# Kernel tuning notes

Measured on AMD Instinct MI355X. Metric: run time of the kernel, lower is better.

Reference implementation:

```python
import jax, jax.numpy as jnp
import numpy as np

BN_EPS = 1e-5

def setup_inputs() -> dict:
    key = jax.random.key(0)
    k1, k2, k3 = jax.random.split(key, 3)
    N, F, H, E = 50000, 256, 256, 1600000
    x = jax.random.normal(k1, (N, F), dtype=jnp.float32)
    edge_index = jax.random.randint(k2, (2, E), 0, N, dtype=jnp.int64)
    # Linear(F, H) params, PyTorch default init scale
    lim = 1.0 / np.sqrt(F)
    W = jax.random.uniform(k3, (H, F), dtype=jnp.float32, minval=-lim, maxval=lim)
    b = jnp.zeros((H,), dtype=jnp.float32)
    bn_w = jnp.ones((H,), dtype=jnp.float32)
    bn_b = jnp.zeros((H,), dtype=jnp.float32)
    return {"x": x, "edge_index": edge_index, "W": W, "b": b, "bn_w": bn_w, "bn_b": bn_b}

def reference(x, edge_index, W, b, bn_w, bn_b):
    N = x.shape[0]
    src, dst = edge_index[0], edge_index[1]
    # GIN aggregation: sum of neighbor features (messages flow src -> dst)
    agg = jax.ops.segment_sum(x[src], dst, num_segments=N)
    h = x + agg  # (1 + eps) * x + agg, eps = 0
    # MLP: Linear then BatchNorm1d (training mode: batch stats, biased var)
    h = jnp.einsum('nf,hf->nh', h, W) + b
    mean = jnp.mean(h, axis=0)
    var = jnp.mean(jnp.square(h - mean), axis=0)
    out = (h - mean) * jax.lax.rsqrt(var + BN_EPS) * bn_w + bn_b
    return out
```

## Files before the change

### kernel.cpp

```cpp
#include <hip/hip_runtime.h>

#define NN 50000
#define FDIM 256
#define HDIM 256
#define BN_EPS 1e-5f
#define RB 32
#define KC 16
#define NP 264
#define SCAN_CHUNK 1024
#define NBLK_SCAN ((NN + SCAN_CHUNK - 1) / SCAN_CHUNK)

#define BKT 32
#define NBKT 1563
#define ECAP 1280
#define CAP 1280
#define SBUF3 13000
#define NFB_MIN 128
#define PSC_NPT 7
#define PAIR_SRC(p) (((p) >> 5) & 0xFFFFu)
#define PAIR_LDST(p) ((p) & 31u)

typedef __attribute__((ext_vector_type(8))) short short8v;
typedef __attribute__((ext_vector_type(8))) unsigned short ushort8v;
typedef __attribute__((ext_vector_type(4))) float f32x4;

__device__ __forceinline__ float b2f(unsigned short u) {
    return __uint_as_float(((unsigned)u) << 16);
}
__device__ __forceinline__ unsigned short f2b(float f) {
    unsigned u = __float_as_uint(f);
    return (unsigned short)((u + 0x7FFFu + ((u >> 16) & 1u)) >> 16);
}

__launch_bounds__(256)
__global__ void k_cvtfill3(const float4* __restrict__ x, const float4* __restrict__ W,
                           ushort4* __restrict__ xb, ushort4* __restrict__ Wb,
                           int nx4, int nw4,
                           const int* __restrict__ src, const int* __restrict__ dst,
                           int* __restrict__ bcnt, unsigned int* __restrict__ pairs,
                           int E, int nfb) {
    const int bid = blockIdx.x;
    const int t = threadIdx.x;
    if (bid >= nfb) {
        int i = (bid - nfb) * 256 + t;
        if (i < nx4) {
            float4 v = x[i];
            xb[i] = make_ushort4(f2b(v.x), f2b(v.y), f2b(v.z), f2b(v.w));
        } else {
            int j = i - nx4;
            if (j < nw4) {
                float4 v = W[j];
                Wb[j] = make_ushort4(f2b(v.x), f2b(v.y), f2b(v.z), f2b(v.w));
            }
        }
        return;
    }
    __shared__ int lhist[NBKT];
    __shared__ int lofs[NBKT];
    __shared__ int ts[256];
    __shared__ unsigned int sbuf[SBUF3];
    const int chunk = (E + nfb - 1) / nfb;
    const int c0 = bid * chunk;
    const int c1 = min(E, c0 + chunk);
    const int n = c1 - c0;

    for (int i = t; i < NBKT; i += 256) lhist[i] = 0;
    __syncthreads();
    for (int e = c0 + t; e < c1; e += 256) atomicAdd(&lhist[dst[e] >> 5], 1);
    __syncthreads();
    {
        int i0 = t * PSC_NPT;
        int s = 0;
        int loc[PSC_NPT];
        for (int i = 0; i < PSC_NPT; i++) {
            int idx = i0 + i;
            loc[i] = (idx < NBKT) ? lhist[idx] : 0;
            s += loc[i];
        }
        ts[t] = s;
        __syncthreads();
        for (int off = 1; off < 256; off <<= 1) {
            int val = (t >= off) ? ts[t - off] : 0;
            __syncthreads();
            ts[t] += val;
            __syncthreads();
        }
        int run = ts[t] - s;
        for (int i = 0; i < PSC_NPT; i++) {
            int idx = i0 + i;
            if (idx < NBKT) {
                lofs[idx] = run;
                run += loc[i];
            }
        }
    }
    __syncthreads();
    for (int i = t; i < NBKT; i += 256) lhist[i] = lofs[i];
    __syncthreads();
    for (int e = c0 + t; e < c1; e += 256) {
        int d = dst[e];
        unsigned bkt = (unsigned)d >> 5;
        int rank = atomicAdd(&lhist[bkt], 1);
        sbuf[rank] = (bkt << 21) | ((unsigned)src[e] << 5) | ((unsigned)d & 31u);
    }
    __syncthreads();
    for (int i = t; i < NBKT; i += 256) {
        int cnt = lhist[i] - lofs[i];
        int gb = cnt ? (i * CAP + atomicAdd(&bcnt[i], cnt)) : 0;
        lhist[i] = gb - lofs[i];
    }
    __syncthreads();
    for (int j = t; j < n; j += 256) {
        unsigned int p = sbuf[j];
        unsigned bkt = p >> 21;
        int pos = j + lhist[bkt];
        if (pos < (int)((bkt + 1) * CAP)) pairs[pos] = p;
    }
}

__launch_bounds__(256, 6)
__global__ void k_agg_gemm(const ushort4* __restrict__ xb4, const unsigned int* __restrict__ pairs,
                           const int* __restrict__ bcnt,
                           const int* __restrict__ srcv, const int* __restrict__ dstv, int E,
                           const unsigned short* __restrict__ Wb, const float* __restrict__ bias,
                           unsigned short* __restrict__ hb, float* __restrict__ stat) {
    __shared__ unsigned int lp[ECAP];
    __shared__ int lhist[BKT];
    __shared__ int lofs[BKT + 1];
    __shared__ unsigned short As[BKT * NP];
    __shared__ float ssum[HDIM];
    __shared__ float ssq[HDIM];
    const int t = threadIdx.x;
    const int lane = t & 63;
    const int wid = t >> 6;
    const int q = lane >> 4;
    const int l16 = lane & 15;
    const int v0 = blockIdx.x * BKT;
    const int ebeg = blockIdx.x * CAP;
    const int ecnt = bcnt[blockIdx.x];
    const int vrows = min(BKT, NN - v0);

    ssum[t] = 0.f;
    ssq[t] = 0.f;

    if (ecnt <= ECAP) {
        if (t < BKT) lhist[t] = 0;
        __syncthreads();
        for (int e = t; e < ecnt; e += 256)
            atomicAdd(&lhist[PAIR_LDST(pairs[ebeg + e])], 1);
        __syncthreads();
        if (t == 0) {
            int run = 0;
            for (int r = 0; r < BKT; r++) { lofs[r] = run; run += lhist[r]; }
            lofs[BKT] = run;
        }
        __syncthreads();
        if (t < BKT) lhist[t] = lofs[t];
        __syncthreads();
        for (int e = t; e < ecnt; e += 256) {
            unsigned int p = pairs[ebeg + e];
            int pos = atomicAdd(&lhist[PAIR_LDST(p)], 1);
            lp[pos] = p;
        }
        __syncthreads();
#pragma unroll
        for (int i = 0; i < 8; i++) {
            int r = wid * 8 + i;
            int v = v0 + r;
            if (v < NN) {
                ushort4 u0 = xb4[(size_t)v * 64 + lane];
                float a0 = b2f(u0.x), a1 = b2f(u0.y), a2 = b2f(u0.z), a3 = b2f(u0.w);
                int e0 = __builtin_amdgcn_readfirstlane(lofs[r]);
                int e1 = __builtin_amdgcn_readfirstlane(lofs[r + 1]);
                int e = e0;
                for (; e + 16 <= e1; e += 16) {
                    ushort4 u[16];
#pragma unroll
                    for (int j = 0; j < 16; j++)
                        u[j] = xb4[(size_t)PAIR_SRC(lp[e + j]) * 64 + lane];
#pragma unroll
                    for (int j = 0; j < 16; j++) {
                        a0 += b2f(u[j].x); a1 += b2f(u[j].y);
                        a2 += b2f(u[j].z); a3 += b2f(u[j].w);
                    }
                }
                for (; e + 4 <= e1; e += 4) {
                    ushort4 ua = xb4[(size_t)PAIR_SRC(lp[e]) * 64 + lane];
                    ushort4 ub = xb4[(size_t)PAIR_SRC(lp[e + 1]) * 64 + lane];
                    ushort4 uc = xb4[(size_t)PAIR_SRC(lp[e + 2]) * 64 + lane];
                    ushort4 ud = xb4[(size_t)PAIR_SRC(lp[e + 3]) * 64 + lane];
                    a0 += (b2f(ua.x) + b2f(ub.x)) + (b2f(uc.x) + b2f(ud.x));
                    a1 += (b2f(ua.y) + b2f(ub.y)) + (b2f(uc.y) + b2f(ud.y));
                    a2 += (b2f(ua.z) + b2f(ub.z)) + (b2f(uc.z) + b2f(ud.z));
                    a3 += (b2f(ua.w) + b2f(ub.w)) + (b2f(uc.w) + b2f(ud.w));
                }
                for (; e < e1; e++) {
                    ushort4 ua = xb4[(size_t)PAIR_SRC(lp[e]) * 64 + lane];
                    a0 += b2f(ua.x); a1 += b2f(ua.y); a2 += b2f(ua.z); a3 += b2f(ua.w);
                }
                *(ushort4*)(As + r * NP + lane * 4) =
                    make_ushort4(f2b(a0), f2b(a1), f2b(a2), f2b(a3));
            } else {
                *(ushort4*)(As + r * NP + lane * 4) = make_ushort4(0, 0, 0, 0);
            }
        }
    } else {
#pragma unroll
        for (int i = 0; i < 8; i++) {
            int r = wid * 8 + i;
            int v = v0 + r;
            float a0 = 0.f, a1 = 0.f, a2 = 0.f, a3 = 0.f;
            if (v < NN) {
                ushort4 u0 = xb4[(size_t)v * 64 + lane];
                a0 = b2f(u0.x); a1 = b2f(u0.y); a2 = b2f(u0.z); a3 = b2f(u0.w);
                for (int e = 0; e < E; e++) {
                    if (dstv[e] == v) {
                        ushort4 cu = xb4[(size_t)srcv[e] * 64 + lane];
                        a0 += b2f(cu.x); a1 += b2f(cu.y); a2 += b2f(cu.z); a3 += b2f(cu.w);
                    }
                }
            }
            *(ushort4*)(As + r * NP + lane * 4) =
                make_ushort4(f2b(a0), f2b(a1), f2b(a2), f2b(a3));
        }
    }
    __syncthreads();

    f32x4 acc[2][4];
#pragma unroll
    for (int mt = 0; mt < 2; mt++)
#pragma unroll
        for (int nt = 0; nt < 4; nt++) acc[mt][nt] = (f32x4)0.f;

    const int w = wid;
#pragma unroll
    for (int ks = 0; ks < 8; ks++) {
        const int kk = ks * 32;
        short8v af[2], bf_[4];
#pragma unroll
        for (int mt = 0; mt < 2; mt++)
            af[mt] = *(const short8v*)(As + (mt * 16 + l16) * NP + kk + q * 8);
#pragma unroll
        for (int nt = 0; nt < 4; nt++)
            bf_[nt] = *(const short8v*)(Wb + (size_t)(w * 64 + nt * 16 + l16) * FDIM + kk + q * 8);
#pragma unroll
        for (int mt = 0; mt < 2; mt++)
#pragma unroll
            for (int nt = 0; nt < 4; nt++)
                acc[mt][nt] = __builtin_amdgcn_mfma_f32_16x16x32_bf16(af[mt], bf_[nt], acc[mt][nt], 0, 0, 0);
    }

#pragma unroll
    for (int nt = 0; nt < 4; nt++) {
        const int col = w * 64 + nt * 16 + l16;
        const float bcol = bias[col];
        float s = 0.f, qq = 0.f;
#pragma unroll
        for (int mt = 0; mt < 2; mt++) {
            const int rbase = mt * 16 + q * 4;
#pragma unroll
            for (int r = 0; r < 4; r++) {
                int row = rbase + r;
                if (row < vrows) {
                    float v = acc[mt][nt][r] + bcol;
                    hb[(size_t)(v0 + row) * FDIM + col] = f2b(v);
                    s += v;
                    qq += v * v;
                }
            }
        }
        atomicAdd(&ssum[col], s);
        atomicAdd(&ssq[col], qq);
    }
    __syncthreads();
    atomicAdd(&stat[t], ssum[t]);
    atomicAdd(&stat[256 + t], ssq[t]);
}

__global__ void k_norm8f(const ushort8v* __restrict__ hb8, const float* __restrict__ stat,
                         const float* __restrict__ bn_w, const float* __restrict__ bn_b,
                         float4* __restrict__ out, int n8) {
    __shared__ float ss[512];
    const int t = threadIdx.x;
    {
        const float inv_n = 1.0f / (float)NN;
        float mean = stat[t] * inv_n;
        float var = stat[256 + t] * inv_n - mean * mean;
        float sc = bn_w[t] * rsqrtf(var + BN_EPS);
        ss[t] = sc;
        ss[256 + t] = bn_b[t] - mean * sc;
    }
    __syncthreads();
    int i = blockIdx.x * 256 + t;
    if (i >= n8) return;
    ushort8v u = hb8[i];
    int c8 = (i & 31) << 3;
    float4 sc0 = *(const float4*)(ss + c8);
    float4 sc1 = *(const float4*)(ss + c8 + 4);
    float4 sh0 = *(const float4*)(ss + 256 + c8);
    float4 sh1 = *(const float4*)(ss + 256 + c8 + 4);
    float4 v0, v1;
    v0.x = fmaf(b2f(u[0]), sc0.x, sh0.x);
    v0.y = fmaf(b2f(u[1]), sc0.y, sh0.y);
    v0.z = fmaf(b2f(u[2]), sc0.z, sh0.z);
    v0.w = fmaf(b2f(u[3]), sc0.w, sh0.w);
    v1.x = fmaf(b2f(u[4]), sc1.x, sh1.x);
    v1.y = fmaf(b2f(u[5]), sc1.y, sh1.y);
    v1.z = fmaf(b2f(u[6]), sc1.z, sh1.z);
    v1.w = fmaf(b2f(u[7]), sc1.w, sh1.w);
    out[i * 2 + 0] = v0;
    out[i * 2 + 1] = v1;
}

__global__ void k_final(const float* __restrict__ stat, const float* __restrict__ bn_w,
                        const float* __restrict__ bn_b, float* __restrict__ ss) {
    int j = threadIdx.x;
    const float inv_n = 1.0f / (float)NN;
    float mean = stat[j] * inv_n;
    float var = stat[256 + j] * inv_n - mean * mean;
    float sc = bn_w[j] * rsqrtf(var + BN_EPS);
    ss[j] = sc;
    ss[256 + j] = bn_b[j] - mean * sc;
}
__global__ void k_hist(const int* __restrict__ dst, int* __restrict__ cnt, int E) {
    int e = blockIdx.x * blockDim.x + threadIdx.x;
    if (e < E) atomicAdd(&cnt[dst[e]], 1);
}
__global__ void k_scan1(const int* __restrict__ cnt, int* __restrict__ offs,
                        int* __restrict__ bsum) {
    __shared__ int ts[256];
    int t = threadIdx.x;
    int base = blockIdx.x * SCAN_CHUNK + t * 4;
    int v0 = (base + 0 < NN) ? cnt[base + 0] : 0;
    int v1 = (base + 1 < NN) ? cnt[base + 1] : 0;
    int v2 = (base + 2 < NN) ? cnt[base + 2] : 0;
    int v3 = (base + 3 < NN) ? cnt[base + 3] : 0;
    int tsum = v0 + v1 + v2 + v3;
    ts[t] = tsum;
    __syncthreads();
    for (int off = 1; off < 256; off <<= 1) {
        int val = (t >= off) ? ts[t - off] : 0;
        __syncthreads();
        ts[t] += val;
        __syncthreads();
    }
    int excl = ts[t] - tsum;
    if (t == 255) bsum[blockIdx.x] = ts[255];
    if (base + 0 < NN) offs[base + 0] = excl;
    if (base + 1 < NN) offs[base + 1] = excl + v0;
    if (base + 2 < NN) offs[base + 2] = excl + v0 + v1;
    if (base + 3 < NN) offs[base + 3] = excl + v0 + v1 + v2;
}
__global__ void k_scan2(int* __restrict__ bsum, int nb) {
    __shared__ int s[64];
    int t = threadIdx.x;
    s[t] = (t < nb) ? bsum[t] : 0;
    __syncthreads();
    if (t == 0) {
        int run = 0;
        for (int i = 0; i < nb; i++) { int v = s[i]; s[i] = run; run += v; }
    }
    __syncthreads();
    if (t < nb) bsum[t] = s[t];
}
__global__ void k_scan3(int* __restrict__ offs, const int* __restrict__ bsum,
                        int* __restrict__ cursor) {
    int i = blockIdx.x * blockDim.x + threadIdx.x;
    if (i >= NN) return;
    int o = offs[i] + bsum[i >> 10];
    offs[i] = o;
    cursor[i] = o;
}
__global__ void k_bucket(const int* __restrict__ src, const int* __restrict__ dst,
                         int* __restrict__ cursor, int* __restrict__ csr, int E) {
    int e = blockIdx.x * blockDim.x + threadIdx.x;
    if (e >= E) return;
    int pos = atomicAdd(&cursor[dst[e]], 1);
    csr[pos] = src[e];
}
__global__ void k_copy(const float4* __restrict__ x, float4* __restrict__ out, int n4) {
    int i = blockIdx.x * blockDim.x + threadIdx.x;
    if (i < n4) out[i] = x[i];
}
__global__ void k_scatter(const float* __restrict__ x, const int* __restrict__ src,
                          const int* __restrict__ dst, float* __restrict__ out, int E) {
    int t = blockIdx.x * blockDim.x + threadIdx.x;
    int e = t >> 6;
    if (e >= E) return;
    int c = (t & 63) << 2;
    long s = src[e], d = dst[e];
    const float4 v = *(const float4*)(x + s * FDIM + c);
    float* o = out + d * FDIM + c;
    atomicAdd(o + 0, v.x);
    atomicAdd(o + 1, v.y);
    atomicAdd(o + 2, v.z);
    atomicAdd(o + 3, v.w);
}
__launch_bounds__(256)
__global__ void k_gather(const float4* __restrict__ x, const int* __restrict__ offs,
                         const int* __restrict__ cnt, const int* __restrict__ csr,
                         float4* __restrict__ out) {
    int v = blockIdx.x * 4 + (threadIdx.x >> 6);
    if (v >= NN) return;
    int lane = threadIdx.x & 63;
    int beg = __builtin_amdgcn_readfirstlane(offs[v]);
    int d   = __builtin_amdgcn_readfirstlane(cnt[v]);
    float4 acc = x[(size_t)v * 64 + lane];
    int i = 0;
    for (; i + 4 <= d; i += 4) {
        int s0 = csr[beg + i], s1 = csr[beg + i + 1];
        int s2 = csr[beg + i + 2], s3 = csr[beg + i + 3];
        float4 a = x[(size_t)s0 * 64 + lane];
        float4 b = x[(size_t)s1 * 64 + lane];
        float4 c = x[(size_t)s2 * 64 + lane];
        float4 e = x[(size_t)s3 * 64 + lane];
        acc.x += (a.x + b.x) + (c.x + e.x);
        acc.y += (a.y + b.y) + (c.y + e.y);
        acc.z += (a.z + b.z) + (c.z + e.z);
        acc.w += (a.w + b.w) + (c.w + e.w);
    }
    for (; i < d; i++) {
        int s = csr[beg + i];
        float4 a = x[(size_t)s * 64 + lane];
        acc.x += a.x; acc.y += a.y; acc.z += a.z; acc.w += a.w;
    }
    out[(size_t)v * 64 + lane] = acc;
}
__launch_bounds__(256)
__global__ void k_gemm_stats(float* __restrict__ h,
                             const float* __restrict__ W,
                             const float* __restrict__ bias,
                             float* __restrict__ stat) {
    __shared__ float hs[RB * FDIM];
    __shared__ float wt[KC * HDIM];
    const int j = threadIdx.x;
    const int c = j & 63;
    const int g = j >> 6;
    const long row0 = (long)blockIdx.x * RB;
    const int vrows = min(RB, NN - (int)row0);
    const int vf4 = vrows * (FDIM / 4);

    float4* hsv = (float4*)hs;
    const float4* hv = (const float4*)(h + row0 * FDIM);
#pragma unroll
    for (int i = 0; i < (RB * FDIM / 4) / 256; i++) {
        int f4 = j + i * 256;
        hsv[f4] = (f4 < vf4) ? hv[f4] : make_float4(0.f, 0.f, 0.f, 0.f);
    }
    __syncthreads();

    float acc[8][4];
#pragma unroll
    for (int r = 0; r < 8; r++)
#pragma unroll
        for (int qi = 0; qi < 4; qi++) acc[r][qi] = 0.f;

    for (int kb = 0; kb < FDIM; kb += KC) {
        __syncthreads();
#pragma unroll
        for (int i = 0; i < KC / 4; i++) {
            float4 w4 = *(const float4*)(W + (size_t)j * FDIM + kb + i * 4);
            wt[(i * 4 + 0) * HDIM + j] = w4.x;
            wt[(i * 4 + 1) * HDIM + j] = w4.y;
            wt[(i * 4 + 2) * HDIM + j] = w4.z;
            wt[(i * 4 + 3) * HDIM + j] = w4.w;
        }
        __syncthreads();
#pragma unroll
        for (int k = 0; k < KC; k++) {
            float4 wv = *(const float4*)(wt + k * HDIM + c * 4);
#pragma unroll
            for (int r = 0; r < 8; r++) {
                float hval = hs[(g * 8 + r) * FDIM + kb + k];
                acc[r][0] = fmaf(hval, wv.x, acc[r][0]);
                acc[r][1] = fmaf(hval, wv.y, acc[r][1]);
                acc[r][2] = fmaf(hval, wv.z, acc[r][2]);
                acc[r][3] = fmaf(hval, wv.w, acc[r][3]);
            }
        }
    }
    __syncthreads();
    wt[j] = 0.f;
    wt[256 + j] = 0.f;
    __syncthreads();

    float4 bv = *(const float4*)(bias + c * 4);
    float s0 = 0, s1 = 0, s2 = 0, s3 = 0, q0 = 0, q1 = 0, q2 = 0, q3 = 0;
#pragma unroll
    for (int r = 0; r < 8; r++) {
        int row = g * 8 + r;
        if (row < vrows) {
            float4 v;
            v.x = acc[r][0] + bv.x;
            v.y = acc[r][1] + bv.y;
            v.z = acc[r][2] + bv.z;
            v.w = acc[r][3] + bv.w;
            *(float4*)(h + (row0 + row) * FDIM + c * 4) = v;
            s0 += v.x; s1 += v.y; s2 += v.z; s3 += v.w;
            q0 += v.x * v.x; q1 += v.y * v.y; q2 += v.z * v.z; q3 += v.w * v.w;
        }
    }
    atomicAdd(&wt[c * 4 + 0], s0);
    atomicAdd(&wt[c * 4 + 1], s1);
    atomicAdd(&wt[c * 4 + 2], s2);
    atomicAdd(&wt[c * 4 + 3], s3);
    atomicAdd(&wt[256 + c * 4 + 0], q0);
    atomicAdd(&wt[256 + c * 4 + 1], q1);
    atomicAdd(&wt[256 + c * 4 + 2], q2);
    atomicAdd(&wt[256 + c * 4 + 3], q3);
    __syncthreads();
    atomicAdd(&stat[j], wt[j]);
    atomicAdd(&stat[256 + j], wt[256 + j]);
}
__global__ void k_norm(float* __restrict__ out, const float* __restrict__ ss, int n4) {
    int i = blockIdx.x * blockDim.x + threadIdx.x;
    if (i >= n4) return;
    float4 v = ((float4*)out)[i];
    int c4 = (i & 63) << 2;
    float4 sc = *(const float4*)(ss + c4);
    float4 sh = *(const float4*)(ss + 256 + c4);
    v.x = fmaf(v.x, sc.x, sh.x);
    v.y = fmaf(v.y, sc.y, sh.y);
    v.z = fmaf(v.z, sc.z, sh.z);
    v.w = fmaf(v.w, sc.w, sh.w);
    ((float4*)out)[i] = v;
}

extern "C" void kernel_launch(void* const* d_in, const int* in_sizes, int n_in,
                              void* d_out, int out_size, void* d_ws, size_t ws_size,
                              hipStream_t stream) {
    const float* x   = (const float*)d_in[0];
    const int*   ei  = (const int*)d_in[1];
    const float* W   = (const float*)d_in[2];
    const float* b   = (const float*)d_in[3];
    const float* bnw = (const float*)d_in[4];
    const float* bnb = (const float*)d_in[5];
    float* out = (float*)d_out;
    char* ws = (char*)d_ws;
    const int E = in_sizes[1] / 2;
    const int n4 = NN * FDIM / 4;
    const int n8 = NN * FDIM / 8;
    const int* src = ei;
    const int* dst = ei + E;

    size_t off = 0;
    float* stat = (float*)(ws + off);          off += 4096;
    int* bcnt   = (int*)(ws + off);            off += 8192;
    unsigned int* pairs = (unsigned int*)(ws + off); off += (size_t)NBKT * CAP * 4;
    off = (off + 255) & ~(size_t)255;
    unsigned short* Wb = (unsigned short*)(ws + off); off += 131072;
    unsigned short* xb = (unsigned short*)(ws + off); off += (size_t)NN * FDIM * 2;
    unsigned short* hb = (unsigned short*)(ws + off); off += (size_t)NN * FDIM * 2;
    const size_t need_fast = off;

    size_t foff = 0;
    float* fstat  = (float*)(ws + foff); foff += 4096;
    int*   cnt    = (int*)(ws + foff);   foff += 204800;
    int*   offs   = (int*)(ws + foff);   foff += 204800;
    int*   cursor = (int*)(ws + foff);   foff += 204800;
    int*   bsum   = (int*)(ws + foff);   foff += 4096;
    int*   csr    = (int*)(ws + foff);   foff += (size_t)E * 4;
    const size_t need_mid = foff;

    const bool src_fits = (NN <= 65536);
    const int nw4 = HDIM * FDIM / 4;

    if (ws_size >= need_fast && src_fits) {
        hipMemsetAsync(ws, 0, 12288, stream);
        int nfb = (E + SBUF3 - 1) / SBUF3;
        if (nfb < NFB_MIN) nfb = NFB_MIN;
        const int ncvt = (n4 + nw4 + 255) / 256;
        k_cvtfill3<<<nfb + ncvt, 256, 0, stream>>>((const float4*)x, (const float4*)W,
                                                   (ushort4*)xb, (ushort4*)Wb, n4, nw4,
                                                   src, dst, bcnt, pairs, E, nfb);
        k_agg_gemm<<<NBKT, 256, 0, stream>>>((const ushort4*)xb, pairs, bcnt,
                                             src, dst, E, Wb, b, hb, stat);
        k_norm8f<<<(n8 + 255) / 256, 256, 0, stream>>>((const ushort8v*)hb, stat,
                                                       bnw, bnb, (float4*)out, n8);
    } else if (ws_size >= need_mid) {
        hipMemsetAsync(fstat, 0, 2 * 256 * sizeof(float), stream);
        hipMemsetAsync(cnt, 0, NN * sizeof(int), stream);
        k_hist<<<(E + 255) / 256, 256, 0, stream>>>(dst, cnt, E);
        k_scan1<<<NBLK_SCAN, 256, 0, stream>>>(cnt, offs, bsum);
        k_scan2<<<1, 64, 0, stream>>>(bsum, NBLK_SCAN);
        k_scan3<<<(NN + 255) / 256, 256, 0, stream>>>(offs, bsum, cursor);
        k_bucket<<<(E + 255) / 256, 256, 0, stream>>>(src, dst, cursor, csr, E);
        k_gather<<<(NN + 3) / 4, 256, 0, stream>>>((const float4*)x, offs, cnt, csr,
                                                   (float4*)out);
        k_gemm_stats<<<(NN + RB - 1) / RB, 256, 0, stream>>>(out, W, b, fstat);
        k_final<<<1, 256, 0, stream>>>(fstat, bnw, bnb, fstat + 512);
        k_norm<<<(n4 + 255) / 256, 256, 0, stream>>>(out, fstat + 512, n4);
    } else {
        hipMemsetAsync(fstat, 0, 2 * 256 * sizeof(float), stream);
        k_copy<<<(n4 + 255) / 256, 256, 0, stream>>>((const float4*)x, (float4*)out, n4);
        long threads = (long)E * 64;
        k_scatter<<<(int)((threads + 255) / 256), 256, 0, stream>>>(x, src, dst, out, E);
        k_gemm_stats<<<(NN + RB - 1) / RB, 256, 0, stream>>>(out, W, b, fstat);
        k_final<<<1, 256, 0, stream>>>(fstat, bnw, bnb, fstat + 512);
        k_norm<<<(n4 + 255) / 256, 256, 0, stream>>>(out, fstat + 512, n4);
    }
}
```

Measured before the change: 320.4 us.

## Split edge bucketing into two halves and overlap second half with aggregation

```diff
diff --git a/kernel.cpp b/kernel.cpp
--- a/kernel.cpp
+++ b/kernel.cpp
@@ -12,11 +12,12 @@
 
 #define BKT 32
 #define NBKT 1563
+#define NBH 782
 #define ECAP 1280
 #define CAP 1280
-#define SBUF3 13000
-#define NFB_MIN 128
-#define PSC_NPT 7
+#define SBUF2 3200
+#define NFB_MIN 512
+#define SMEM_INTS 6144
 #define PAIR_SRC(p) (((p) >> 5) & 0xFFFFu)
 #define PAIR_LDST(p) ((p) & 31u)
 
@@ -32,49 +33,37 @@
     return (unsigned short)((u + 0x7FFFu + ((u >> 16) & 1u)) >> 16);
 }
 
-__launch_bounds__(256)
-__global__ void k_cvtfill3(const float4* __restrict__ x, const float4* __restrict__ W,
-                           ushort4* __restrict__ xb, ushort4* __restrict__ Wb,
-                           int nx4, int nw4,
-                           const int* __restrict__ src, const int* __restrict__ dst,
-                           int* __restrict__ bcnt, unsigned int* __restrict__ pairs,
-                           int E, int nfb) {
-    const int bid = blockIdx.x;
+__device__ __forceinline__ void fill_range(int cid, int nfb, int* smem,
+                                           const int* __restrict__ src,
+                                           const int* __restrict__ dst,
+                                           int* __restrict__ bcnt,
+                                           unsigned int* __restrict__ pairs,
+                                           int E, int bkt_lo, int bkt_hi) {
+    int* lhist = smem;
+    int* lofs  = smem + 800;
+    int* ts    = smem + 1600;
+    unsigned int* sbuf = (unsigned int*)(smem + 1856);
     const int t = threadIdx.x;
-    if (bid >= nfb) {
-        int i = (bid - nfb) * 256 + t;
-        if (i < nx4) {
-            float4 v = x[i];
-            xb[i] = make_ushort4(f2b(v.x), f2b(v.y), f2b(v.z), f2b(v.w));
-        } else {
-            int j = i - nx4;
-            if (j < nw4) {
-                float4 v = W[j];
-                Wb[j] = make_ushort4(f2b(v.x), f2b(v.y), f2b(v.z), f2b(v.w));
-            }
-        }
-        return;
-    }
-    __shared__ int lhist[NBKT];
-    __shared__ int lofs[NBKT];
-    __shared__ int ts[256];
-    __shared__ unsigned int sbuf[SBUF3];
+    const int nbh = bkt_hi - bkt_lo;
     const int chunk = (E + nfb - 1) / nfb;
-    const int c0 = bid * chunk;
+    const int c0 = cid * chunk;
     const int c1 = min(E, c0 + chunk);
-    const int n = c1 - c0;
-
-    for (int i = t; i < NBKT; i += 256) lhist[i] = 0;
-    __syncthreads();
-    for (int e = c0 + t; e < c1; e += 256) atomicAdd(&lhist[dst[e] >> 5], 1);
-    __syncthreads();
+
+    for (int i = t; i < nbh; i += 256) lhist[i] = 0;
+    __syncthreads();
+    for (int e = c0 + t; e < c1; e += 256) {
+        int b = dst[e] >> 5;
+        if (b >= bkt_lo && b < bkt_hi) atomicAdd(&lhist[b - bkt_lo], 1);
+    }
+    __syncthreads();
+    int ntot;
     {
-        int i0 = t * PSC_NPT;
+        int i0 = t * 4;
         int s = 0;
-        int loc[PSC_NPT];
-        for (int i = 0; i < PSC_NPT; i++) {
+        int loc[4];
+        for (int i = 0; i < 4; i++) {
             int idx = i0 + i;
-            loc[i] = (idx < NBKT) ? lhist[idx] : 0;
+            loc[i] = (idx < nbh) ? lhist[idx] : 0;
             s += loc[i];
         }
         ts[t] = s;
@@ -86,58 +75,66 @@
             __syncthreads();
         }
         int run = ts[t] - s;
-        for (int i = 0; i < PSC_NPT; i++) {
+        for (int i = 0; i < 4; i++) {
             int idx = i0 + i;
-            if (idx < NBKT) {
+            if (idx < nbh) {
                 lofs[idx] = run;
                 run += loc[i];
             }
         }
-    }
-    __syncthreads();
-    for (int i = t; i < NBKT; i += 256) lhist[i] = lofs[i];
+        ntot = ts[255];
+    }
+    __syncthreads();
+    for (int i = t; i < nbh; i += 256) lhist[i] = lofs[i];
     __syncthreads();
     for (int e = c0 + t; e < c1; e += 256) {
         int d = dst[e];
-        unsigned bkt = (unsigned)d >> 5;
-        int rank = atomicAdd(&lhist[bkt], 1);
-        sbuf[rank] = (bkt << 21) | ((unsigned)src[e] << 5) | ((unsigned)d & 31u);
-    }
-    __syncthreads();
-    for (int i = t; i < NBKT; i += 256) {
+        int b = d >> 5;
+        if (b >= bkt_lo && b < bkt_hi) {
+            unsigned bl = (unsigned)(b - bkt_lo);
+            int rank = atomicAdd(&lhist[bl], 1);
+            sbuf[rank] = (bl << 21) | ((unsigned)src[e] << 5) | ((unsigned)d & 31u);
+        }
+    }
+    __syncthreads();
+    for (int i = t; i < nbh; i += 256) {
         int cnt = lhist[i] - lofs[i];
-        int gb = cnt ? (i * CAP + atomicAdd(&bcnt[i], cnt)) : 0;
+        int gb = cnt ? ((bkt_lo + i) * CAP + atomicAdd(&bcnt[bkt_lo + i], cnt)) : 0;
         lhist[i] = gb - lofs[i];
     }
     __syncthreads();
-    for (int j = t; j < n; j += 256) {
+    for (int j = t; j < ntot; j += 256) {
         unsigned int p = sbuf[j];
-        unsigned bkt = p >> 21;
-        int pos = j + lhist[bkt];
-        if (pos < (int)((bkt + 1) * CAP)) pairs[pos] = p;
-    }
-}
-
-__launch_bounds__(256, 6)
-__global__ void k_agg_gemm(const ushort4* __restrict__ xb4, const unsigned int* __restrict__ pairs,
-                           const int* __restrict__ bcnt,
-                           const int* __restrict__ srcv, const int* __restrict__ dstv, int E,
-                           const unsigned short* __restrict__ Wb, const float* __restrict__ bias,
-                           unsigned short* __restrict__ hb, float* __restrict__ stat) {
-    __shared__ unsigned int lp[ECAP];
-    __shared__ int lhist[BKT];
-    __shared__ int lofs[BKT + 1];
-    __shared__ unsigned short As[BKT * NP];
-    __shared__ float ssum[HDIM];
-    __shared__ float ssq[HDIM];
+        unsigned bl = p >> 21;
+        int pos = j + lhist[bl];
+        if (pos < (int)((bkt_lo + bl + 1) * CAP)) pairs[pos] = p;
+    }
+}
+
+__device__ __forceinline__ void agg_bucket(int bkt, int* smem,
+                                           const ushort4* __restrict__ xb4,
+                                           const unsigned int* __restrict__ pairs,
+                                           const int* __restrict__ bcnt,
+                                           const int* __restrict__ srcv,
+                                           const int* __restrict__ dstv, int E,
+                                           const unsigned short* __restrict__ Wb,
+                                           const float* __restrict__ bias,
+                                           unsigned short* __restrict__ hb,
+                                           float* __restrict__ stat) {
+    unsigned int* lp = (unsigned int*)smem;
+    int* lhist = smem + 1280;
+    int* lofs  = smem + 1312;
+    unsigned short* As = (unsigned short*)(smem + 1346);
+    float* ssum = (float*)(smem + 5570);
+    float* ssq  = (float*)(smem + 5826);
     const int t = threadIdx.x;
     const int lane = t & 63;
     const int wid = t >> 6;
     const int q = lane >> 4;
     const int l16 = lane & 15;
-    const int v0 = blockIdx.x * BKT;
-    const int ebeg = blockIdx.x * CAP;
-    const int ecnt = bcnt[blockIdx.x];
+    const int v0 = bkt * BKT;
+    const int ebeg = bkt * CAP;
+    const int ecnt = bcnt[bkt];
     const int vrows = min(BKT, NN - v0);
 
     ssum[t] = 0.f;
@@ -277,6 +274,57 @@
     atomicAdd(&stat[256 + t], ssq[t]);
 }
 
+__launch_bounds__(256, 6)
+__global__ void k_cvtfillA(const float4* __restrict__ x, const float4* __restrict__ W,
+                           ushort4* __restrict__ xb, ushort4* __restrict__ Wb,
+                           int nx4, int nw4,
+                           const int* __restrict__ src, const int* __restrict__ dst,
+                           int* __restrict__ bcnt, unsigned int* __restrict__ pairs,
+                           int E, int nfb) {
+    __shared__ int smem[SMEM_INTS];
+    const int bid = blockIdx.x;
+    if (bid < nfb) {
+        fill_range(bid, nfb, smem, src, dst, bcnt, pairs, E, 0, NBH);
+        return;
+    }
+    int i = (bid - nfb) * 256 + threadIdx.x;
+    if (i < nx4) {
+        float4 v = x[i];
+        xb[i] = make_ushort4(f2b(v.x), f2b(v.y), f2b(v.z), f2b(v.w));
+    } else {
+        int j = i - nx4;
+        if (j < nw4) {
+            float4 v = W[j];
+            Wb[j] = make_ushort4(f2b(v.x), f2b(v.y), f2b(v.z), f2b(v.w));
+        }
+    }
+}
+
+__launch_bounds__(256, 6)
+__global__ void k_mix(const ushort4* __restrict__ xb4, const unsigned int* __restrict__ pairs,
+                      int* __restrict__ bcnt,
+                      const int* __restrict__ src, const int* __restrict__ dst, int E,
+                      const unsigned short* __restrict__ Wb, const float* __restrict__ bias,
+                      unsigned short* __restrict__ hb, float* __restrict__ stat, int nfb) {
+    __shared__ int smem[SMEM_INTS];
+    const int bid = blockIdx.x;
+    if (bid < nfb) {
+        fill_range(bid, nfb, smem, src, dst, bcnt, (unsigned int*)pairs, E, NBH, NBKT);
+        return;
+    }
+    agg_bucket(bid - nfb, smem, xb4, pairs, bcnt, src, dst, E, Wb, bias, hb, stat);
+}
+
+__launch_bounds__(256, 6)
+__global__ void k_aggB(const ushort4* __restrict__ xb4, const unsigned int* __restrict__ pairs,
+                       const int* __restrict__ bcnt,
+                       const int* __restrict__ src, const int* __restrict__ dst, int E,
+                       const unsigned short* __restrict__ Wb, const float* __restrict__ bias,
+                       unsigned short* __restrict__ hb, float* __restrict__ stat) {
+    __shared__ int smem[SMEM_INTS];
+    agg_bucket(NBH + blockIdx.x, smem, xb4, pairs, bcnt, src, dst, E, Wb, bias, hb, stat);
+}
+
 __global__ void k_norm8f(const ushort8v* __restrict__ hb8, const float* __restrict__ stat,
                          const float* __restrict__ bn_w, const float* __restrict__ bn_b,
                          float4* __restrict__ out, int n8) {
@@ -567,14 +615,16 @@
 
     if (ws_size >= need_fast && src_fits) {
         hipMemsetAsync(ws, 0, 12288, stream);
-        int nfb = (E + SBUF3 - 1) / SBUF3;
+        int nfb = (E + SBUF2 - 1) / SBUF2;
         if (nfb < NFB_MIN) nfb = NFB_MIN;
         const int ncvt = (n4 + nw4 + 255) / 256;
-        k_cvtfill3<<<nfb + ncvt, 256, 0, stream>>>((const float4*)x, (const float4*)W,
+        k_cvtfillA<<<nfb + ncvt, 256, 0, stream>>>((const float4*)x, (const float4*)W,
                                                    (ushort4*)xb, (ushort4*)Wb, n4, nw4,
                                                    src, dst, bcnt, pairs, E, nfb);
-        k_agg_gemm<<<NBKT, 256, 0, stream>>>((const ushort4*)xb, pairs, bcnt,
-                                             src, dst, E, Wb, b, hb, stat);
+        k_mix<<<nfb + NBH, 256, 0, stream>>>((const ushort4*)xb, pairs, bcnt,
+                                             src, dst, E, Wb, b, hb, stat, nfb);
+        k_aggB<<<NBKT - NBH, 256, 0, stream>>>((const ushort4*)xb, pairs, bcnt,
+                                               src, dst, E, Wb, b, hb, stat);
         k_norm8f<<<(n8 + 255) / 256, 256, 0, stream>>>((const ushort8v*)hb, stat,
                                                        bnw, bnb, (float4*)out, n8);
     } else if (ws_size >= need_mid) {
```

Result: slower. 346.6 us (+8.2%).
